# Performance work log

Measured on AMD Instinct MI355X. Metric: run time of the kernel, lower is better.

## Reference

```python
import jax, jax.numpy as jnp
import numpy as np


def setup_inputs() -> dict:
    key = jax.random.key(0)
    k1, k2, k3, k4, k5 = jax.random.split(key, 5)
    dim, hidden = 64, 128
    x = jax.random.normal(k1, (32, 128, 128, dim), dtype=jnp.float32)
    # torch Linear stores (out,in); we store transposed so y = x @ W + b
    W_expand = jax.random.normal(k2, (dim, hidden), dtype=jnp.float32) * (1.0 / np.sqrt(dim))
    b_expand = jax.random.normal(k3, (hidden,), dtype=jnp.float32) * 0.01
    W_restore = jax.random.normal(k4, (hidden, 1), dtype=jnp.float32) * (1.0 / np.sqrt(hidden))
    b_restore = jax.random.normal(k5, (1,), dtype=jnp.float32) * 0.01
    return {
        "x": x,
        "W_expand": W_expand,
        "b_expand": b_expand,
        "W_restore": W_restore,
        "b_restore": b_restore,
        "kernel_size": 2,
        "stride": 2,
    }


def reference(x, W_expand, b_expand, W_restore, b_restore, kernel_size, stride):
    b, r, c, d = x.shape
    sr = (r - kernel_size) // stride + 1
    sc = (c - kernel_size) // stride + 1
    s = stride  # original code slices stride x stride windows
    # gather all windows at once: (b, sr, s, sc, s, d)
    ri = (jnp.arange(sr) * stride)[:, None] + jnp.arange(s)[None, :]
    ci = (jnp.arange(sc) * stride)[:, None] + jnp.arange(s)[None, :]
    win = x[:, ri[:, :, None, None], ci[None, None, :, :], :]
    # -> (b, sr, sc, s*s, d)
    win = win.transpose(0, 1, 3, 2, 4, 5).reshape(b, sr, sc, s * s, d)
    # tiny MLP attention weights per window element
    h = jnp.tanh(jnp.einsum('bqpwd,dh->bqpwh', win, W_expand) + b_expand)
    logit = jax.nn.sigmoid(jnp.einsum('bqpwh,ho->bqpwo', h, W_restore)[..., 0] + b_restore[0])
    w = jax.nn.softmax(logit, axis=-1)  # over window elements
    out = jnp.sum(win * w[..., None], axis=3)  # (b, sr, sc, d)
    return out
```

## Files before the change

### kernel.cpp

```cpp
#include <hip/hip_runtime.h>


typedef __attribute__((ext_vector_type(8))) short short8;
typedef __attribute__((ext_vector_type(4))) float floatx4;

#define B_   32
#define R_   128
#define C_   128
#define D_   64
#define H_   128
#define SR_  64
#define SC_  64
#define NW_  (B_ * SR_ * SC_)
#define NGRP_ (NW_ / 4)
#define NBLK_ 2048
#define NWAVE_ (NBLK_ * 4)
#define L_   (NGRP_ / NWAVE_)
#define WTS_ 72

#define L2E_  1.4426950408889634f
#define T2L_  2.8853900817779268f

__device__ __forceinline__ unsigned short f2bf_rne(float f) {
  union { float f; unsigned int u; } v; v.f = f;
  unsigned int u = v.u;
  u += 0x7fffu + ((u >> 16) & 1u);
  return (unsigned short)(u >> 16);
}

__device__ __forceinline__ unsigned int pk_bf16(float lo, float hi) {
  union { float f; unsigned int u; } a, b; a.f = lo; b.f = hi;
  return ((a.u + 0x8000u) >> 16) | ((b.u + 0x8000u) & 0xFFFF0000u);
}

template <int CTRL>
__device__ __forceinline__ float dpp_add(float x) {
  int xi = __builtin_bit_cast(int, x);
  int yi = __builtin_amdgcn_update_dpp(0, xi, CTRL, 0xf, 0xf, true);
  return x + __builtin_bit_cast(float, yi);
}
#define DPP_XOR1   0xB1
#define DPP_XOR3   0x1B
#define DPP_XOR7   0x141
#define DPP_XOR15  0x140

__device__ __forceinline__ float row_reduce16(float x) {
  x = dpp_add<DPP_XOR1>(x);
  x = dpp_add<DPP_XOR3>(x);
  x = dpp_add<DPP_XOR7>(x);
  x = dpp_add<DPP_XOR15>(x);
  return x;
}

__global__ __launch_bounds__(256, 2) void softpool_kernel(
    const float* __restrict__ x, const float* __restrict__ We,
    const float* __restrict__ be, const float* __restrict__ Wr,
    const float* __restrict__ br, float* __restrict__ out)
{
  __shared__ __attribute__((aligned(16))) unsigned short WeT[H_ * WTS_];

  const int tid = threadIdx.x;
  for (int idx = tid; idx < D_ * H_; idx += 256) {
    int d = idx >> 7;
    int h = idx & 127;
    WeT[h * WTS_ + d] = f2bf_rne(We[idx]);
  }
  __syncthreads();

  const int lane = tid & 63;
  const int wv   = tid >> 6;
  const int c    = lane & 15;
  const int quad = lane >> 4;

  short8 Bf[8][2];
#pragma unroll
  for (int n = 0; n < 8; ++n)
#pragma unroll
    for (int ks = 0; ks < 2; ++ks)
      Bf[n][ks] = *(const short8*)&WeT[(n * 16 + c) * WTS_ + ks * 32 + quad * 8];

  float beK[8], wr2[8], swr = 0.f;
#pragma unroll
  for (int n = 0; n < 8; ++n) {
    float w = Wr[n * 16 + c];
    beK[n] = be[n * 16 + c] * T2L_;
    wr2[n] = -2.0f * w;
    swr += w;
  }
  const float brN = -L2E_ * br[0];

  const int gw = blockIdx.x * 4 + wv;

  for (int it = 0; it < L_; ++it) {
    const int g = gw + it * NWAVE_;

    const int w0   = g * 4 + (c >> 2);
    const int elem = c & 3;
    const int bb = w0 >> 12;
    const int qq = (w0 >> 6) & 63;
    const int pp = w0 & 63;
    const int row = qq * 2 + (elem >> 1);
    const int col = pp * 2 + (elem & 1);
    const float* xp = x + (((bb * R_ + row) * C_ + col) * D_) + quad * 8;

    const int wq = g * 4 + quad;
    const int b2 = wq >> 12;
    const int q2 = (wq >> 6) & 63;
    const int p2i = wq & 63;
    const float* xw = x + (((b2 * R_ + q2 * 2) * C_ + p2i * 2) * D_) + c * 4;

    floatx4 a0 = *(const floatx4*)(xp);
    floatx4 a1 = *(const floatx4*)(xp + 4);
    floatx4 a2 = *(const floatx4*)(xp + 32);
    floatx4 a3 = *(const floatx4*)(xp + 36);
    floatx4 x0 = *(const floatx4*)(xw);
    floatx4 x1 = *(const floatx4*)(xw + D_);
    floatx4 x2 = *(const floatx4*)(xw + C_ * D_);
    floatx4 x3 = *(const floatx4*)(xw + C_ * D_ + D_);

    union { unsigned int u[4]; short8 v; } A0u, A1u;
    A0u.u[0] = pk_bf16(a0[0], a0[1]); A0u.u[1] = pk_bf16(a0[2], a0[3]);
    A0u.u[2] = pk_bf16(a1[0], a1[1]); A0u.u[3] = pk_bf16(a1[2], a1[3]);
    A1u.u[0] = pk_bf16(a2[0], a2[1]); A1u.u[1] = pk_bf16(a2[2], a2[3]);
    A1u.u[2] = pk_bf16(a3[0], a3[1]); A1u.u[3] = pk_bf16(a3[2], a3[3]);

    floatx4 acc[8];
#pragma unroll
    for (int n = 0; n < 8; ++n) {
      floatx4 z = {0.f, 0.f, 0.f, 0.f};
      z = __builtin_amdgcn_mfma_f32_16x16x32_bf16(A0u.v, Bf[n][0], z, 0, 0, 0);
      acc[n] = __builtin_amdgcn_mfma_f32_16x16x32_bf16(A1u.v, Bf[n][1], z, 0, 0, 0);
    }

    float p0 = swr, p1 = swr, p2 = swr, p3 = swr;
#pragma unroll
    for (int n = 0; n < 8; ++n) {
      float e0 = __builtin_amdgcn_exp2f(fmaf(acc[n][0], T2L_, beK[n]));
      float e1 = __builtin_amdgcn_exp2f(fmaf(acc[n][1], T2L_, beK[n]));
      float e2 = __builtin_amdgcn_exp2f(fmaf(acc[n][2], T2L_, beK[n]));
      float e3 = __builtin_amdgcn_exp2f(fmaf(acc[n][3], T2L_, beK[n]));
      p0 = fmaf(wr2[n], __builtin_amdgcn_rcpf(e0 + 1.0f), p0);
      p1 = fmaf(wr2[n], __builtin_amdgcn_rcpf(e1 + 1.0f), p1);
      p2 = fmaf(wr2[n], __builtin_amdgcn_rcpf(e2 + 1.0f), p2);
      p3 = fmaf(wr2[n], __builtin_amdgcn_rcpf(e3 + 1.0f), p3);
    }
    p0 = row_reduce16(p0);
    p1 = row_reduce16(p1);
    p2 = row_reduce16(p2);
    p3 = row_reduce16(p3);
    float l0 = __builtin_amdgcn_rcpf(1.0f + __builtin_amdgcn_exp2f(fmaf(p0, -L2E_, brN)));
    float l1 = __builtin_amdgcn_rcpf(1.0f + __builtin_amdgcn_exp2f(fmaf(p1, -L2E_, brN)));
    float l2 = __builtin_amdgcn_rcpf(1.0f + __builtin_amdgcn_exp2f(fmaf(p2, -L2E_, brN)));
    float l3 = __builtin_amdgcn_rcpf(1.0f + __builtin_amdgcn_exp2f(fmaf(p3, -L2E_, brN)));
    float s0 = __builtin_amdgcn_exp2f(l0 * L2E_);
    float s1 = __builtin_amdgcn_exp2f(l1 * L2E_);
    float s2 = __builtin_amdgcn_exp2f(l2 * L2E_);
    float s3 = __builtin_amdgcn_exp2f(l3 * L2E_);
    float inv = __builtin_amdgcn_rcpf(s0 + s1 + s2 + s3);
    float w0f = s0 * inv, w1f = s1 * inv, w2f = s2 * inv, w3f = s3 * inv;

    floatx4 o = x0 * w0f + x1 * w1f + x2 * w2f + x3 * w3f;
    *(floatx4*)(out + wq * 64 + c * 4) = o;
  }
}

extern "C" void kernel_launch(void* const* d_in, const int* in_sizes, int n_in,
                              void* d_out, int out_size, void* d_ws, size_t ws_size,
                              hipStream_t stream) {
  const float* x  = (const float*)d_in[0];
  const float* We = (const float*)d_in[1];
  const float* be = (const float*)d_in[2];
  const float* Wr = (const float*)d_in[3];
  const float* br = (const float*)d_in[4];
  float* out = (float*)d_out;
  softpool_kernel<<<NBLK_, 256, 0, stream>>>(x, We, be, Wr, br, out);
}
```

Baseline: 216.2 us.

## Pre-pack bf16 weight fragments in a prep kernel and launch one block per group

```diff
diff --git a/kernel.cpp b/kernel.cpp
--- a/kernel.cpp
+++ b/kernel.cpp
@@ -9,14 +9,9 @@
 #define C_   128
 #define D_   64
 #define H_   128
-#define SR_  64
-#define SC_  64
-#define NW_  (B_ * SR_ * SC_)
+#define NW_  (B_ * 64 * 64)
 #define NGRP_ (NW_ / 4)
-#define NBLK_ 2048
-#define NWAVE_ (NBLK_ * 4)
-#define L_   (NGRP_ / NWAVE_)
-#define WTS_ 72
+#define NBLK_ (NGRP_ / 4)
 
 #define L2E_  1.4426950408889634f
 #define T2L_  2.8853900817779268f
@@ -29,8 +24,9 @@
 }
 
 __device__ __forceinline__ unsigned int pk_bf16(float lo, float hi) {
-  union { float f; unsigned int u; } a, b; a.f = lo; b.f = hi;
-  return ((a.u + 0x8000u) >> 16) | ((b.u + 0x8000u) & 0xFFFF0000u);
+  unsigned int a = __builtin_bit_cast(unsigned int, lo) + 0x8000u;
+  unsigned int b = __builtin_bit_cast(unsigned int, hi) + 0x8000u;
+  return __builtin_amdgcn_perm(b, a, 0x07060302u);
 }
 
 template <int CTRL>
@@ -43,7 +39,6 @@
 #define DPP_XOR3   0x1B
 #define DPP_XOR7   0x141
 #define DPP_XOR15  0x140
-
 __device__ __forceinline__ float row_reduce16(float x) {
   x = dpp_add<DPP_XOR1>(x);
   x = dpp_add<DPP_XOR3>(x);
@@ -52,32 +47,58 @@
   return x;
 }
 
+__global__ void prep_kernel(const float* __restrict__ We,
+                            unsigned short* __restrict__ F)
+{
+  int t = blockIdx.x * 256 + threadIdx.x;
+  int j    = t & 7;
+  int lane = (t >> 3) & 63;
+  int fi   = t >> 9;
+  int n  = fi >> 1, ks = fi & 1;
+  int quad = lane >> 4, c = lane & 15;
+  F[t] = f2bf_rne(We[(ks * 32 + quad * 8 + j) * 128 + n * 16 + c]);
+}
+
 __global__ __launch_bounds__(256, 2) void softpool_kernel(
-    const float* __restrict__ x, const float* __restrict__ We,
+    const float* __restrict__ x, const unsigned short* __restrict__ F,
     const float* __restrict__ be, const float* __restrict__ Wr,
     const float* __restrict__ br, float* __restrict__ out)
 {
-  __shared__ __attribute__((aligned(16))) unsigned short WeT[H_ * WTS_];
-
-  const int tid = threadIdx.x;
-  for (int idx = tid; idx < D_ * H_; idx += 256) {
-    int d = idx >> 7;
-    int h = idx & 127;
-    WeT[h * WTS_ + d] = f2bf_rne(We[idx]);
-  }
-  __syncthreads();
-
-  const int lane = tid & 63;
-  const int wv   = tid >> 6;
+  const int lane = threadIdx.x & 63;
+  const int wv   = threadIdx.x >> 6;
   const int c    = lane & 15;
   const int quad = lane >> 4;
+
+  const int g = blockIdx.x * 4 + wv;
 
   short8 Bf[8][2];
 #pragma unroll
   for (int n = 0; n < 8; ++n)
 #pragma unroll
     for (int ks = 0; ks < 2; ++ks)
-      Bf[n][ks] = *(const short8*)&WeT[(n * 16 + c) * WTS_ + ks * 32 + quad * 8];
+      Bf[n][ks] = *(const short8*)&F[((n * 2 + ks) * 64 + lane) * 8];
+
+  const int w0   = g * 4 + (c >> 2);
+  const int elem = c & 3;
+  const int bb = w0 >> 12;
+  const int qq = (w0 >> 6) & 63;
+  const int pp = w0 & 63;
+  const float* xp = x + (((bb * R_ + (qq * 2 + (elem >> 1))) * C_
+                          + (pp * 2 + (elem & 1))) * D_) + quad * 8;
+  floatx4 a0 = *(const floatx4*)(xp);
+  floatx4 a1 = *(const floatx4*)(xp + 4);
+  floatx4 a2 = *(const floatx4*)(xp + 32);
+  floatx4 a3 = *(const floatx4*)(xp + 36);
+
+  const int wq = g * 4 + quad;
+  const int b2 = wq >> 12;
+  const int q2 = (wq >> 6) & 63;
+  const int p2i = wq & 63;
+  const float* xw = x + (((b2 * R_ + q2 * 2) * C_ + p2i * 2) * D_) + c * 4;
+  floatx4 x0 = *(const floatx4*)(xw);
+  floatx4 x1 = *(const floatx4*)(xw + D_);
+  floatx4 x2 = *(const floatx4*)(xw + C_ * D_);
+  floatx4 x3 = *(const floatx4*)(xw + C_ * D_ + D_);
 
   float beK[8], wr2[8], swr = 0.f;
 #pragma unroll
@@ -89,79 +110,49 @@
   }
   const float brN = -L2E_ * br[0];
 
-  const int gw = blockIdx.x * 4 + wv;
+  union { unsigned int u[4]; short8 v; } A0u, A1u;
+  A0u.u[0] = pk_bf16(a0[0], a0[1]); A0u.u[1] = pk_bf16(a0[2], a0[3]);
+  A0u.u[2] = pk_bf16(a1[0], a1[1]); A0u.u[3] = pk_bf16(a1[2], a1[3]);
+  A1u.u[0] = pk_bf16(a2[0], a2[1]); A1u.u[1] = pk_bf16(a2[2], a2[3]);
+  A1u.u[2] = pk_bf16(a3[0], a3[1]); A1u.u[3] = pk_bf16(a3[2], a3[3]);
 
-  for (int it = 0; it < L_; ++it) {
-    const int g = gw + it * NWAVE_;
+  floatx4 acc[8];
+#pragma unroll
+  for (int n = 0; n < 8; ++n) {
+    floatx4 z = {0.f, 0.f, 0.f, 0.f};
+    z = __builtin_amdgcn_mfma_f32_16x16x32_bf16(A0u.v, Bf[n][0], z, 0, 0, 0);
+    acc[n] = __builtin_amdgcn_mfma_f32_16x16x32_bf16(A1u.v, Bf[n][1], z, 0, 0, 0);
+  }
 
-    const int w0   = g * 4 + (c >> 2);
-    const int elem = c & 3;
-    const int bb = w0 >> 12;
-    const int qq = (w0 >> 6) & 63;
-    const int pp = w0 & 63;
-    const int row = qq * 2 + (elem >> 1);
-    const int col = pp * 2 + (elem & 1);
-    const float* xp = x + (((bb * R_ + row) * C_ + col) * D_) + quad * 8;
+  float p0 = swr, p1 = swr, p2 = swr, p3 = swr;
+#pragma unroll
+  for (int n = 0; n < 8; ++n) {
+    float e0 = __builtin_amdgcn_exp2f(fmaf(acc[n][0], T2L_, beK[n]));
+    float e1 = __builtin_amdgcn_exp2f(fmaf(acc[n][1], T2L_, beK[n]));
+    float e2 = __builtin_amdgcn_exp2f(fmaf(acc[n][2], T2L_, beK[n]));
+    float e3 = __builtin_amdgcn_exp2f(fmaf(acc[n][3], T2L_, beK[n]));
+    p0 = fmaf(wr2[n], __builtin_amdgcn_rcpf(e0 + 1.0f), p0);
+    p1 = fmaf(wr2[n], __builtin_amdgcn_rcpf(e1 + 1.0f), p1);
+    p2 = fmaf(wr2[n], __builtin_amdgcn_rcpf(e2 + 1.0f), p2);
+    p3 = fmaf(wr2[n], __builtin_amdgcn_rcpf(e3 + 1.0f), p3);
+  }
+  p0 = row_reduce16(p0);
+  p1 = row_reduce16(p1);
+  p2 = row_reduce16(p2);
+  p3 = row_reduce16(p3);
+  float l0 = __builtin_amdgcn_rcpf(1.0f + __builtin_amdgcn_exp2f(fmaf(p0, -L2E_, brN)));
+  float l1 = __builtin_amdgcn_rcpf(1.0f + __builtin_amdgcn_exp2f(fmaf(p1, -L2E_, brN)));
+  float l2 = __builtin_amdgcn_rcpf(1.0f + __builtin_amdgcn_exp2f(fmaf(p2, -L2E_, brN)));
+  float l3 = __builtin_amdgcn_rcpf(1.0f + __builtin_amdgcn_exp2f(fmaf(p3, -L2E_, brN)));
+  float s0 = __builtin_amdgcn_exp2f(l0 * L2E_);
+  float s1 = __builtin_amdgcn_exp2f(l1 * L2E_);
+  float s2 = __builtin_amdgcn_exp2f(l2 * L2E_);
+  float s3 = __builtin_amdgcn_exp2f(l3 * L2E_);
+  float inv = __builtin_amdgcn_rcpf(s0 + s1 + s2 + s3);
+  float w0f = s0 * inv, w1f = s1 * inv, w2f = s2 * inv, w3f = s3 * inv;
 
-    const int wq = g * 4 + quad;
-    const int b2 = wq >> 12;
-    const int q2 = (wq >> 6) & 63;
-    const int p2i = wq & 63;
-    const float* xw = x + (((b2 * R_ + q2 * 2) * C_ + p2i * 2) * D_) + c * 4;
-
-    floatx4 a0 = *(const floatx4*)(xp);
-    floatx4 a1 = *(const floatx4*)(xp + 4);
-    floatx4 a2 = *(const floatx4*)(xp + 32);
-    floatx4 a3 = *(const floatx4*)(xp + 36);
-    floatx4 x0 = *(const floatx4*)(xw);
-    floatx4 x1 = *(const floatx4*)(xw + D_);
-    floatx4 x2 = *(const floatx4*)(xw + C_ * D_);
-    floatx4 x3 = *(const floatx4*)(xw + C_ * D_ + D_);
-
-    union { unsigned int u[4]; short8 v; } A0u, A1u;
-    A0u.u[0] = pk_bf16(a0[0], a0[1]); A0u.u[1] = pk_bf16(a0[2], a0[3]);
-    A0u.u[2] = pk_bf16(a1[0], a1[1]); A0u.u[3] = pk_bf16(a1[2], a1[3]);
-    A1u.u[0] = pk_bf16(a2[0], a2[1]); A1u.u[1] = pk_bf16(a2[2], a2[3]);
-    A1u.u[2] = pk_bf16(a3[0], a3[1]); A1u.u[3] = pk_bf16(a3[2], a3[3]);
-
-    floatx4 acc[8];
-#pragma unroll
-    for (int n = 0; n < 8; ++n) {
-      floatx4 z = {0.f, 0.f, 0.f, 0.f};
-      z = __builtin_amdgcn_mfma_f32_16x16x32_bf16(A0u.v, Bf[n][0], z, 0, 0, 0);
-      acc[n] = __builtin_amdgcn_mfma_f32_16x16x32_bf16(A1u.v, Bf[n][1], z, 0, 0, 0);
-    }
-
-    float p0 = swr, p1 = swr, p2 = swr, p3 = swr;
-#pragma unroll
-    for (int n = 0; n < 8; ++n) {
-      float e0 = __builtin_amdgcn_exp2f(fmaf(acc[n][0], T2L_, beK[n]));
-      float e1 = __builtin_amdgcn_exp2f(fmaf(acc[n][1], T2L_, beK[n]));
-      float e2 = __builtin_amdgcn_exp2f(fmaf(acc[n][2], T2L_, beK[n]));
-      float e3 = __builtin_amdgcn_exp2f(fmaf(acc[n][3], T2L_, beK[n]));
-      p0 = fmaf(wr2[n], __builtin_amdgcn_rcpf(e0 + 1.0f), p0);
-      p1 = fmaf(wr2[n], __builtin_amdgcn_rcpf(e1 + 1.0f), p1);
-      p2 = fmaf(wr2[n], __builtin_amdgcn_rcpf(e2 + 1.0f), p2);
-      p3 = fmaf(wr2[n], __builtin_amdgcn_rcpf(e3 + 1.0f), p3);
-    }
-    p0 = row_reduce16(p0);
-    p1 = row_reduce16(p1);
-    p2 = row_reduce16(p2);
-    p3 = row_reduce16(p3);
-    float l0 = __builtin_amdgcn_rcpf(1.0f + __builtin_amdgcn_exp2f(fmaf(p0, -L2E_, brN)));
-    float l1 = __builtin_amdgcn_rcpf(1.0f + __builtin_amdgcn_exp2f(fmaf(p1, -L2E_, brN)));
-    float l2 = __builtin_amdgcn_rcpf(1.0f + __builtin_amdgcn_exp2f(fmaf(p2, -L2E_, brN)));
-    float l3 = __builtin_amdgcn_rcpf(1.0f + __builtin_amdgcn_exp2f(fmaf(p3, -L2E_, brN)));
-    float s0 = __builtin_amdgcn_exp2f(l0 * L2E_);
-    float s1 = __builtin_amdgcn_exp2f(l1 * L2E_);
-    float s2 = __builtin_amdgcn_exp2f(l2 * L2E_);
-    float s3 = __builtin_amdgcn_exp2f(l3 * L2E_);
-    float inv = __builtin_amdgcn_rcpf(s0 + s1 + s2 + s3);
-    float w0f = s0 * inv, w1f = s1 * inv, w2f = s2 * inv, w3f = s3 * inv;
-
-    floatx4 o = x0 * w0f + x1 * w1f + x2 * w2f + x3 * w3f;
-    *(floatx4*)(out + wq * 64 + c * 4) = o;
-  }
+  floatx4 o = x0 * w0f + x1 * w1f + x2 * w2f + x3 * w3f;
+  *(floatx4*)(out + (long)wq * 64 + c * 4) = o;
 }
 
 extern "C" void kernel_launch(void* const* d_in, const int* in_sizes, int n_in,
@@ -173,5 +164,8 @@
   const float* Wr = (const float*)d_in[3];
   const float* br = (const float*)d_in[4];
   float* out = (float*)d_out;
-  softpool_kernel<<<NBLK_, 256, 0, stream>>>(x, We, be, Wr, br, out);
+  unsigned short* F = (unsigned short*)d_ws;
+
+  prep_kernel<<<32, 256, 0, stream>>>(We, F);
+  softpool_kernel<<<NBLK_, 256, 0, stream>>>(x, F, be, Wr, br, out);
 }
```

Result: no change. 217.4 us (+0.6%).
